# Optimization experiments

Hardware: AMD Instinct MI355X
Metric: run time of the kernel (lower is better)

The kernel has to match this reference:

```python
import jax, jax.numpy as jnp
import numpy as np

B, D, K, NC, F = 2048, 256, 256, 64, 512
EPS = 1e-3           # transport_eps
TAU_MIN = 0.01
TAU_DENOM_MIN = 1e-3


def setup_inputs() -> dict:
    key = jax.random.key(0)
    ks = jax.random.split(key, 8)
    # latents strictly inside the Poincare ball (norm ~0.5 for D=256)
    z = 0.03 * jax.random.normal(ks[0], (B, D), jnp.float32)
    features = jax.random.normal(ks[1], (B, F), jnp.float32)
    # SpectralLinear params (treated as plain linear layers in the reference)
    W_qz = 0.02 * jax.random.normal(ks[2], (K, D), jnp.float32)
    b_qz = jnp.zeros((K,), jnp.float32)
    W_qf = 0.02 * jax.random.normal(ks[3], (K, F), jnp.float32)
    b_qf = jnp.zeros((K,), jnp.float32)
    # full tensorization gamma: [K, D, D]
    q_gamma = 0.02 * jax.random.normal(ks[4], (K, D, D), jnp.float32)
    chart_queries = 0.02 * jax.random.normal(ks[5], (NC, K), jnp.float32)
    return {
        "z": z, "features": features,
        "W_qz": W_qz, "b_qz": b_qz, "W_qf": W_qf, "b_qf": b_qf,
        "q_gamma": q_gamma, "chart_queries": chart_queries,
    }


def reference(z, features, W_qz, b_qz, W_qf, b_qf, q_gamma, chart_queries):
    # centers = chart_queries[:, :latent_dim] (chart_tokens=None path); D == K here
    centers = chart_queries[:, :D]                      # [NC, D]

    # ---- hyperbolic (Poincare ball) distance scores ----
    r2 = jnp.sum(z * z, axis=-1)                        # [B]
    c_sq = jnp.sum(centers * centers, axis=-1)          # [NC]
    diff = z[:, None, :] - centers[None, :, :]          # [B, NC, D]
    dist_sq = jnp.sum(diff * diff, axis=-1)             # [B, NC]
    denom = (1.0 - r2[:, None]) * (1.0 - c_sq[None, :])
    arg = 1.0 + 2.0 * dist_sq / (denom + EPS)
    dist = jnp.arccosh(jnp.maximum(arg, 1.0 + EPS))

    # metric-aware temperature tau(z)
    tau = jnp.maximum(
        jnp.sqrt(jnp.float32(K)) * jnp.maximum(1.0 - r2, TAU_DENOM_MIN) * 0.5,
        TAU_MIN,
    )                                                   # [B]
    scores = -dist / tau[:, None]                       # [B, NC]

    # ---- feature-based refinement (q_feat_proj branch) ----
    q = z @ W_qz.T + b_qz + features @ W_qf.T + b_qf    # [B, K]
    # gamma term: einsum('bij,kij->bk', z outer z, q_gamma) without [B,D,D]
    gz = jnp.einsum('bj,kij->bki', z, q_gamma)          # [B, K, D]
    q = q + jnp.einsum('bki,bi->bk', gz, z)             # [B, K]

    # transported queries: base_queries / lambda(z); (Q/lam) . q == (q @ Q.T)/lam
    r2c = jnp.minimum(r2, 1.0 - EPS)
    lam = 2.0 / (1.0 - r2c + EPS)                       # [B]
    feature_scores = (q @ chart_queries.T) / lam[:, None]  # [B, NC]

    scores = scores + 0.1 * feature_scores / tau[:, None]

    router_weights = jax.nn.softmax(scores, axis=-1)    # [B, NC]
    K_chart = jnp.argmax(router_weights, axis=-1)       # [B]
    return router_weights, K_chart
```

## Files before the change

kernel.cpp:

```cpp
#include <hip/hip_runtime.h>
#include <hip/hip_bf16.h>
#include <hip/hip_fp16.h>


#define B_SZ 2048
#define D_SZ 256
#define K_SZ 256
#define NC_SZ 64
#define F_SZ 512
#define P_SZ 65536

typedef float  floatx4  __attribute__((ext_vector_type(4)));
typedef float  floatx16 __attribute__((ext_vector_type(16)));
typedef _Float16 h8 __attribute__((ext_vector_type(8)));
typedef __fp16  fp16x2 __attribute__((ext_vector_type(2)));
union H8U4 { uint4 u; h8 h; };

#define WS_WZT   0
#define WS_WFT   16384
#define WS_BEFF  49152
#define WS_CSQ   49216
#define WS_CQT   49280
#define WS_Q2    65664
#define WS_MH    196736
#define WS_WALL  2293888
#define WS_PART  2351232

__device__ __forceinline__ unsigned pkrtz_u(float a, float b) {
    fp16x2 r = __builtin_amdgcn_cvt_pkrtz(a, b);
    return __builtin_bit_cast(unsigned, r);
}
__device__ __forceinline__ unsigned packh2(_Float16 a, _Float16 b) {
    union { _Float16 h[2]; unsigned u; } r; r.h[0] = a; r.h[1] = b; return r.u;
}
__device__ __forceinline__ unsigned packh(float a, float b) {
    return packh2((_Float16)a, (_Float16)b);
}

__device__ __forceinline__ void gload16(const void* g, void* l) {
    __builtin_amdgcn_global_load_lds(
        (const __attribute__((address_space(1))) unsigned*)g,
        (__attribute__((address_space(3))) unsigned*)l, 16, 0, 0);
}

__global__ __launch_bounds__(256) void prep_kernel(
        const float* __restrict__ Wqz, const float* __restrict__ bqz,
        const float* __restrict__ Wqf, const float* __restrict__ bqf,
        const float* __restrict__ cq,  float* __restrict__ ws) {
    const int tid = threadIdx.x;
    const int w = tid >> 6, c = tid & 63;
    const int bid = blockIdx.x;

    if (bid >= 193) {
        _Float16* cqh = (_Float16*)(ws + WS_Q2);
        const int idx = (bid - 193)*256 + tid;
        const floatx4* sp = (const floatx4*)(cq + idx*8);
        floatx4 a = sp[0], b = sp[1];
        uint4 u = { pkrtz_u(a[0],a[1]), pkrtz_u(a[2],a[3]),
                    pkrtz_u(b[0],b[1]), pkrtz_u(b[2],b[3]) };
        *(uint4*)(cqh + idx*8) = u;
        return;
    }

    __shared__ float cqL[64*257];
    #pragma unroll
    for (int s = 0; s < 16; ++s) {
        const int e4 = s*256 + tid;
        const int row = e4 >> 6, col = (e4 & 63)*4;
        floatx4 v = *(const floatx4*)(cq + e4*4);
        #pragma unroll
        for (int u = 0; u < 4; ++u) cqL[row*257 + col + u] = v[u];
    }
    __syncthreads();

    if (bid < 64) {
        const int i = bid*4 + w;
        float a0 = 0.f, a1 = 0.f, a2 = 0.f, a3 = 0.f;
        #pragma unroll 8
        for (int k = 0; k < K_SZ; k += 4) {
            a0 = fmaf(cqL[c*257 + k    ], Wqz[(k    )*D_SZ + i], a0);
            a1 = fmaf(cqL[c*257 + k + 1], Wqz[(k + 1)*D_SZ + i], a1);
            a2 = fmaf(cqL[c*257 + k + 2], Wqz[(k + 2)*D_SZ + i], a2);
            a3 = fmaf(cqL[c*257 + k + 3], Wqz[(k + 3)*D_SZ + i], a3);
        }
        ws[WS_WZT + i*64 + c] = (a0 + a1) + (a2 + a3);
        ws[WS_CQT + i*64 + c] = cqL[c*257 + i];
    } else if (bid < 192) {
        const int j = (bid - 64)*4 + w;
        float a0 = 0.f, a1 = 0.f, a2 = 0.f, a3 = 0.f;
        #pragma unroll 8
        for (int k = 0; k < K_SZ; k += 4) {
            a0 = fmaf(cqL[c*257 + k    ], Wqf[(k    )*F_SZ + j], a0);
            a1 = fmaf(cqL[c*257 + k + 1], Wqf[(k + 1)*F_SZ + j], a1);
            a2 = fmaf(cqL[c*257 + k + 2], Wqf[(k + 2)*F_SZ + j], a2);
            a3 = fmaf(cqL[c*257 + k + 3], Wqf[(k + 3)*F_SZ + j], a3);
        }
        ws[WS_WFT + j*64 + c] = (a0 + a1) + (a2 + a3);
    } else {
        if (w == 0) {
            float acc = 0.f;
            for (int k = 0; k < K_SZ; ++k)
                acc = fmaf(cqL[c*257 + k], bqz[k] + bqf[k], acc);
            ws[WS_BEFF + c] = acc;
        } else if (w == 1) {
            float acc = 0.f;
            for (int i = 0; i < D_SZ; ++i) {
                const float v = cqL[c*257 + i];
                acc = fmaf(v, v, acc);
            }
            ws[WS_CSQ + c] = acc;
        }
    }
}

__global__ __launch_bounds__(256) void prep2_kernel(float* __restrict__ ws) {
    const int gi = blockIdx.x*256 + threadIdx.x;
    const int s  = gi >> 11, e = gi & 2047;
    const int cr = e >> 5,  u = e & 31;
    const float* __restrict__ src =
        (s == 0) ? ws + WS_WZT :
        (s <= 2) ? ws + WS_WFT :
        (s <= 4) ? ws + WS_WFT + 16384 : ws + WS_CQT;
    const bool lo = (s == 2) || (s == 4) || (s == 6);
    float v[8];
    #pragma unroll
    for (int off = 0; off < 8; ++off)
        v[off] = src[(u*8 + off)*64 + cr];
    uint4 o;
    if (!lo) {
        o.x = packh(v[0], v[1]); o.y = packh(v[2], v[3]);
        o.z = packh(v[4], v[5]); o.w = packh(v[6], v[7]);
    } else {
        float l[8];
        #pragma unroll
        for (int off = 0; off < 8; ++off) {
            const _Float16 h = (_Float16)v[off];
            l[off] = (v[off] - (float)h) * 1024.f;
        }
        o.x = pkrtz_u(l[0], l[1]); o.y = pkrtz_u(l[2], l[3]);
        o.z = pkrtz_u(l[4], l[5]); o.w = pkrtz_u(l[6], l[7]);
    }
    char* wall = (char*)(ws + WS_WALL);
    *(uint4*)(wall + s*32768 + cr*512 + ((u ^ (cr & 31)) << 4)) = o;
}

__global__ __launch_bounds__(256, 4) void mc_kernel(
        const float* __restrict__ gamma, const _Float16* __restrict__ cqh,
        _Float16* __restrict__ mh) {
    const int tid = threadIdx.x;
    const int w = tid >> 6, lane = tid & 63;
    const int ln = lane & 31, half = lane >> 5;
    const int mt = w >> 1, ns = w & 1;
    const int p0 = blockIdx.x * 64;
    const int iseg = p0 >> 8, j0 = p0 & 255;

    floatx16 acc;
    #pragma unroll
    for (int r = 0; r < 16; ++r) acc[r] = 0.f;

    const int arow = mt*32 + ln;
    const float* __restrict__ gbase = gamma + (size_t)(half*8)*P_SZ + p0 + ns*32 + ln;

    #pragma unroll 2
    for (int kc = 0; kc < 16; ++kc) {
        float g[8];
        #pragma unroll
        for (int kk = 0; kk < 8; ++kk)
            g[kk] = gbase[(size_t)(kc*16 + kk)*P_SZ];
        H8U4 a; a.u = *(const uint4*)(cqh + arow*256 + kc*16 + half*8);
        H8U4 b;
        b.u.x = pkrtz_u(g[0], g[1]);
        b.u.y = pkrtz_u(g[2], g[3]);
        b.u.z = pkrtz_u(g[4], g[5]);
        b.u.w = pkrtz_u(g[6], g[7]);
        acc = __builtin_amdgcn_mfma_f32_32x32x16_f16(a.h, b.h, acc, 0, 0, 0);
    }
    #pragma unroll
    for (int r = 0; r < 16; ++r) {
        const int cc = mt*32 + (r&3) + 8*(r>>2) + 4*half;
        const int j  = j0 + ns*32 + ln;
        const int jc = j >> 3, off = j & 7;
        mh[(size_t)cc*P_SZ + iseg*256 + ((jc ^ (cc&31))*8 + off)] = (_Float16)acc[r];
    }
}

__global__ __launch_bounds__(256) void qf_kernel(
        const float* __restrict__ z, const _Float16* __restrict__ mh,
        float* __restrict__ part) {
    __shared__ __align__(16) char bt[2][64 * 512];
    const int tid = threadIdx.x;
    const int w = tid >> 6, lane = tid & 63;
    const int ln = lane & 31, half = lane >> 5;
    const int b0 = blockIdx.x * 128;
    const int ig = blockIdx.y;
    const int bb = b0 + w*32 + ln;

    #define STAGE(i, sel)                                                     \
        _Pragma("unroll")                                                     \
        for (int s = 0; s < 8; ++s) {                                         \
            const int e = s*256 + tid;                                        \
            gload16((const char*)mh +                                         \
                    ((size_t)(e >> 5)*P_SZ + (size_t)(i)*256)*2 + (e & 31)*16,\
                    bt[sel] + e*16);                                          \
        }

    STAGE(ig*8, 0);

    uint4 zjh[16];
    #pragma unroll
    for (int ch = 0; ch < 16; ++ch) {
        const floatx4* zp = (const floatx4*)(z + bb*D_SZ + ch*16 + half*8);
        floatx4 a = zp[0], b = zp[1];
        zjh[ch].x = pkrtz_u(a[0], a[1]);
        zjh[ch].y = pkrtz_u(a[2], a[3]);
        zjh[ch].z = pkrtz_u(b[0], b[1]);
        zjh[ch].w = pkrtz_u(b[2], b[3]);
    }
    float ziv[8];
    {
        const floatx4* zp = (const floatx4*)(z + bb*D_SZ + ig*8);
        floatx4 a = zp[0], b = zp[1];
        #pragma unroll
        for (int t = 0; t < 4; ++t) { ziv[t] = a[t]; ziv[4+t] = b[t]; }
    }

    floatx16 acc0, acc1;
    #pragma unroll
    for (int r = 0; r < 16; ++r) { acc0[r] = 0.f; acc1[r] = 0.f; }

    for (int il = 0; il < 8; ++il) {
        __syncthreads();
        if (il < 7) { STAGE(ig*8 + il + 1, (il + 1) & 1); }

        const float zi = ziv[il];
        const unsigned zu = pkrtz_u(zi, zi);
        H8U4 zb; zb.u.x = zu; zb.u.y = zu; zb.u.z = zu; zb.u.w = zu;
        const char* btc = bt[il & 1];
        __builtin_amdgcn_s_setprio(1);
        #pragma unroll
        for (int ch = 0; ch < 16; ++ch) {
            H8U4 aj; aj.u = zjh[ch];
            h8 af = aj.h * zb.h;
            const int pc = ((ch*2 + half) ^ ln) * 16;
            H8U4 f0, f1;
            f0.u = *(const uint4*)(btc + ln*512 + pc);
            f1.u = *(const uint4*)(btc + (32 + ln)*512 + pc);
            acc0 = __builtin_amdgcn_mfma_f32_32x32x16_f16(af, f0.h, acc0, 0, 0, 0);
            acc1 = __builtin_amdgcn_mfma_f32_32x32x16_f16(af, f1.h, acc1, 0, 0, 0);
        }
        __builtin_amdgcn_s_setprio(0);
    }
    #undef STAGE

    float* __restrict__ qp = part + (size_t)ig * (B_SZ * NC_SZ);
    #pragma unroll
    for (int r = 0; r < 16; ++r) {
        const int row  = (r&3) + 8*(r>>2) + 4*half;
        const int brow = b0 + w*32 + row;
        qp[brow*NC_SZ + ln]      = acc0[r];
        qp[brow*NC_SZ + 32 + ln] = acc1[r];
    }
}

__global__ __launch_bounds__(256) void lin2_kernel(
        const float* __restrict__ z, const float* __restrict__ feat,
        const float* __restrict__ wall_f, float* __restrict__ part,
        float* __restrict__ dot) {
    __shared__ __align__(16) char bt[2][64 * 512];
    const char* wall = (const char*)wall_f;
    const int tid = threadIdx.x;
    const int w = tid >> 6, lane = tid & 63;
    const int ln = lane & 31, half = lane >> 5;
    const int b0 = blockIdx.x * 128;
    const int s  = blockIdx.y;
    const int bb = b0 + w*32 + ln;
    const int s_hi = (s == 0) ? 0 : (s == 1) ? 1 : (s == 2) ? 3 : 5;

    #pragma unroll
    for (int e0 = 0; e0 < 8; ++e0) {
        const int e = e0*256 + tid;
        gload16(wall + s_hi*32768 + e*16, bt[0] + e*16);
    }
    if (s > 0) {
        #pragma unroll
        for (int e0 = 0; e0 < 8; ++e0) {
            const int e = e0*256 + tid;
            gload16(wall + (s_hi + 1)*32768 + e*16, bt[1] + e*16);
        }
    }
    const float* __restrict__ arow =
        (s == 0 || s == 3) ? z + bb*D_SZ : feat + bb*F_SZ + (s == 2 ? 256 : 0);
    __syncthreads();

    floatx16 hh0, hh1, lh0, lh1, hl0, hl1;
    #pragma unroll
    for (int r = 0; r < 16; ++r) {
        hh0[r] = 0.f; hh1[r] = 0.f; lh0[r] = 0.f;
        lh1[r] = 0.f; hl0[r] = 0.f; hl1[r] = 0.f;
    }

    #pragma unroll
    for (int ch = 0; ch < 16; ++ch) {
        const floatx4* ap = (const floatx4*)(arow + ch*16 + half*8);
        floatx4 a4 = ap[0], b4 = ap[1];
        float vv[8];
        #pragma unroll
        for (int t = 0; t < 4; ++t) { vv[t] = a4[t]; vv[4+t] = b4[t]; }
        _Float16 hc[8];
        #pragma unroll
        for (int j = 0; j < 8; ++j) hc[j] = (_Float16)vv[j];
        H8U4 ah;
        ah.u.x = packh2(hc[0], hc[1]); ah.u.y = packh2(hc[2], hc[3]);
        ah.u.z = packh2(hc[4], hc[5]); ah.u.w = packh2(hc[6], hc[7]);

        const int pc = ((ch*2 + half) ^ ln) * 16;
        H8U4 f0, f1;
        f0.u = *(const uint4*)(bt[0] + ln*512 + pc);
        f1.u = *(const uint4*)(bt[0] + (32 + ln)*512 + pc);
        hh0 = __builtin_amdgcn_mfma_f32_32x32x16_f16(ah.h, f0.h, hh0, 0, 0, 0);
        hh1 = __builtin_amdgcn_mfma_f32_32x32x16_f16(ah.h, f1.h, hh1, 0, 0, 0);

        if (s > 0) {
            float l[8];
            #pragma unroll
            for (int j = 0; j < 8; ++j) l[j] = (vv[j] - (float)hc[j]) * 1024.f;
            H8U4 al;
            al.u.x = pkrtz_u(l[0], l[1]); al.u.y = pkrtz_u(l[2], l[3]);
            al.u.z = pkrtz_u(l[4], l[5]); al.u.w = pkrtz_u(l[6], l[7]);
            H8U4 g0, g1;
            g0.u = *(const uint4*)(bt[1] + ln*512 + pc);
            g1.u = *(const uint4*)(bt[1] + (32 + ln)*512 + pc);
            lh0 = __builtin_amdgcn_mfma_f32_32x32x16_f16(al.h, f0.h, lh0, 0, 0, 0);
            lh1 = __builtin_amdgcn_mfma_f32_32x32x16_f16(al.h, f1.h, lh1, 0, 0, 0);
            hl0 = __builtin_amdgcn_mfma_f32_32x32x16_f16(ah.h, g0.h, hl0, 0, 0, 0);
            hl1 = __builtin_amdgcn_mfma_f32_32x32x16_f16(ah.h, g1.h, hl1, 0, 0, 0);
        }
    }

    const float is = 1.0f / 1024.0f;
    float* __restrict__ qp = part + (size_t)(32 + s) * (B_SZ * NC_SZ);
    #pragma unroll
    for (int r = 0; r < 16; ++r) {
        const int row  = (r&3) + 8*(r>>2) + 4*half;
        const int brow = b0 + w*32 + row;
        float v0 = hh0[r], v1 = hh1[r];
        if (s > 0) { v0 += (lh0[r] + hl0[r])*is; v1 += (lh1[r] + hl1[r])*is; }
        if (s < 3) {
            qp[brow*NC_SZ + ln]      = v0;
            qp[brow*NC_SZ + 32 + ln] = v1;
        } else {
            dot[brow*NC_SZ + ln]      = v0;
            dot[brow*NC_SZ + 32 + ln] = v1;
        }
    }
}

__global__ __launch_bounds__(256) void final_kernel(
        const float* __restrict__ z, const float* __restrict__ ws,
        const float* __restrict__ dot, float* __restrict__ out) {
    const int w = threadIdx.x >> 6, c = threadIdx.x & 63;
    const int b = blockIdx.x*4 + w;

    const floatx4 zv = *(const floatx4*)(z + b*D_SZ + c*4);
    float r2 = zv[0]*zv[0] + zv[1]*zv[1] + zv[2]*zv[2] + zv[3]*zv[3];
    #pragma unroll
    for (int off = 32; off > 0; off >>= 1)
        r2 += __shfl_xor(r2, off, 64);

    const float* __restrict__ part = ws + WS_PART;
    float Q = ws[WS_BEFF + c];
    #pragma unroll
    for (int p = 0; p < 35; ++p)
        Q += part[(size_t)p * (B_SZ*NC_SZ) + b*NC_SZ + c];

    const float csq = ws[WS_CSQ + c];
    const float dsq = fmaf(-2.f, dot[b*64 + c], r2) + csq;

    const double r2d = (double)r2, csqd = (double)csq, dsqd = (double)dsq;
    const double denom = (1.0 - r2d) * (1.0 - csqd);
    double arg = 1.0 + 2.0 * dsqd / (denom + 0.001);
    if (arg < 1.001) arg = 1.001;
    const double dist = acosh(arg);
    double tmp = 1.0 - r2d; if (tmp < 0.001) tmp = 0.001;
    double tau = 8.0 * tmp;
    if (tau < 0.01) tau = 0.01;
    double r2c = r2d; if (r2c > 0.999) r2c = 0.999;
    const double lam = 2.0 / (1.0 - r2c + 0.001);
    const double score = -dist / tau + 0.1 * ((double)Q / lam) / tau;

    double m = score;
    #pragma unroll
    for (int off = 32; off > 0; off >>= 1) {
        double o = __shfl_xor(m, off, 64);
        m = fmax(m, o);
    }
    const double e = exp(score - m);
    double s = e;
    #pragma unroll
    for (int off = 32; off > 0; off >>= 1) s += __shfl_xor(s, off, 64);
    out[b*NC_SZ + c] = (float)(e / s);

    double bsc = score; int bix = c;
    #pragma unroll
    for (int off = 32; off > 0; off >>= 1) {
        double osc = __shfl_xor(bsc, off, 64);
        int    oix = __shfl_xor(bix, off, 64);
        if (osc > bsc || (osc == bsc && oix < bix)) { bsc = osc; bix = oix; }
    }
    if (c == 0) out[B_SZ*NC_SZ + b] = (float)bix;
}

extern "C" void kernel_launch(void* const* d_in, const int* in_sizes, int n_in,
                              void* d_out, int out_size, void* d_ws, size_t ws_size,
                              hipStream_t stream) {
    const float* z    = (const float*)d_in[0];
    const float* feat = (const float*)d_in[1];
    const float* Wqz  = (const float*)d_in[2];
    const float* bqz  = (const float*)d_in[3];
    const float* Wqf  = (const float*)d_in[4];
    const float* bqf  = (const float*)d_in[5];
    const float* gamma= (const float*)d_in[6];
    const float* cq   = (const float*)d_in[7];
    float* out = (float*)d_out;
    float* ws  = (float*)d_ws;
    _Float16* cqh = (_Float16*)(ws + WS_Q2);
    _Float16* mh  = (_Float16*)(ws + WS_MH);
    float*    dot = ws + WS_MH;

    prep_kernel<<<201, 256, 0, stream>>>(Wqz, bqz, Wqf, bqf, cq, ws);
    prep2_kernel<<<56, 256, 0, stream>>>(ws);
    mc_kernel<<<1024, 256, 0, stream>>>(gamma, cqh, mh);
    qf_kernel<<<dim3(16, 32), 256, 0, stream>>>(z, mh, ws + WS_PART);
    lin2_kernel<<<dim3(16, 4), 256, 0, stream>>>(z, feat, ws + WS_WALL,
                                                 ws + WS_PART, dot);
    final_kernel<<<512, 256, 0, stream>>>(z, ws, dot, out);
}
```

Before: 177.0 us.

## Fuse fp16 weight packing into prep kernel and remap blocks for XCD locality

Removes the prep2 kernel by having prep_kernel write the fp16 hi/lo split, swizzled weight layout straight into the WALL buffer, which saves a launch and a round trip through the fp32 intermediates. The mc_kernel K-loop now starts at a per-block rotated offset so concurrent blocks spread their gamma reads across different rows. qf_kernel switches to a 1D grid mapped so blocks sharing an i-group land on the same XCD, aiming for better L2 reuse of mh tiles. The fused writes are scattered 2-byte stores instead of packed 16-byte stores.

```diff
diff --git a/kernel.cpp b/kernel.cpp
--- a/kernel.cpp
+++ b/kernel.cpp
@@ -16,11 +16,8 @@
 typedef __fp16  fp16x2 __attribute__((ext_vector_type(2)));
 union H8U4 { uint4 u; h8 h; };
 
-#define WS_WZT   0
-#define WS_WFT   16384
 #define WS_BEFF  49152
 #define WS_CSQ   49216
-#define WS_CQT   49280
 #define WS_Q2    65664
 #define WS_MH    196736
 #define WS_WALL  2293888
@@ -30,11 +27,12 @@
     fp16x2 r = __builtin_amdgcn_cvt_pkrtz(a, b);
     return __builtin_bit_cast(unsigned, r);
 }
+__device__ __forceinline__ _Float16 h16rtz(float x) {
+    fp16x2 r = __builtin_amdgcn_cvt_pkrtz(x, x);
+    return (_Float16)r[0];
+}
 __device__ __forceinline__ unsigned packh2(_Float16 a, _Float16 b) {
     union { _Float16 h[2]; unsigned u; } r; r.h[0] = a; r.h[1] = b; return r.u;
-}
-__device__ __forceinline__ unsigned packh(float a, float b) {
-    return packh2((_Float16)a, (_Float16)b);
 }
 
 __device__ __forceinline__ void gload16(const void* g, void* l) {
@@ -50,6 +48,7 @@
     const int tid = threadIdx.x;
     const int w = tid >> 6, c = tid & 63;
     const int bid = blockIdx.x;
+    char* wall = (char*)(ws + WS_WALL);
 
     if (bid >= 193) {
         _Float16* cqh = (_Float16*)(ws + WS_Q2);
@@ -83,8 +82,14 @@
             a2 = fmaf(cqL[c*257 + k + 2], Wqz[(k + 2)*D_SZ + i], a2);
             a3 = fmaf(cqL[c*257 + k + 3], Wqz[(k + 3)*D_SZ + i], a3);
         }
-        ws[WS_WZT + i*64 + c] = (a0 + a1) + (a2 + a3);
-        ws[WS_CQT + i*64 + c] = cqL[c*257 + i];
+        const float acc = (a0 + a1) + (a2 + a3);
+        const int boff = c*512 + ((((i >> 3) & 31) ^ (c & 31)) << 4) + (i & 7)*2;
+        *(_Float16*)(wall + 0*32768 + boff) = (_Float16)acc;
+        const float v = cqL[c*257 + i];
+        const _Float16 vh = (_Float16)v;
+        *(_Float16*)(wall + 5*32768 + boff) = vh;
+        *(_Float16*)(wall + 6*32768 + boff) =
+            h16rtz((v - (float)vh) * 1024.f);
     } else if (bid < 192) {
         const int j = (bid - 64)*4 + w;
         float a0 = 0.f, a1 = 0.f, a2 = 0.f, a3 = 0.f;
@@ -95,7 +100,14 @@
             a2 = fmaf(cqL[c*257 + k + 2], Wqf[(k + 2)*F_SZ + j], a2);
             a3 = fmaf(cqL[c*257 + k + 3], Wqf[(k + 3)*F_SZ + j], a3);
         }
-        ws[WS_WFT + j*64 + c] = (a0 + a1) + (a2 + a3);
+        const float acc = (a0 + a1) + (a2 + a3);
+        const int row = j & 255;
+        const int sbase = (j < 256) ? 1 : 3;
+        const int boff = c*512 + ((((row >> 3) & 31) ^ (c & 31)) << 4) + (row & 7)*2;
+        const _Float16 ah = (_Float16)acc;
+        *(_Float16*)(wall + (size_t)sbase*32768 + boff) = ah;
+        *(_Float16*)(wall + (size_t)(sbase + 1)*32768 + boff) =
+            h16rtz((acc - (float)ah) * 1024.f);
     } else {
         if (w == 0) {
             float acc = 0.f;
@@ -113,37 +125,6 @@
     }
 }
 
-__global__ __launch_bounds__(256) void prep2_kernel(float* __restrict__ ws) {
-    const int gi = blockIdx.x*256 + threadIdx.x;
-    const int s  = gi >> 11, e = gi & 2047;
-    const int cr = e >> 5,  u = e & 31;
-    const float* __restrict__ src =
-        (s == 0) ? ws + WS_WZT :
-        (s <= 2) ? ws + WS_WFT :
-        (s <= 4) ? ws + WS_WFT + 16384 : ws + WS_CQT;
-    const bool lo = (s == 2) || (s == 4) || (s == 6);
-    float v[8];
-    #pragma unroll
-    for (int off = 0; off < 8; ++off)
-        v[off] = src[(u*8 + off)*64 + cr];
-    uint4 o;
-    if (!lo) {
-        o.x = packh(v[0], v[1]); o.y = packh(v[2], v[3]);
-        o.z = packh(v[4], v[5]); o.w = packh(v[6], v[7]);
-    } else {
-        float l[8];
-        #pragma unroll
-        for (int off = 0; off < 8; ++off) {
-            const _Float16 h = (_Float16)v[off];
-            l[off] = (v[off] - (float)h) * 1024.f;
-        }
-        o.x = pkrtz_u(l[0], l[1]); o.y = pkrtz_u(l[2], l[3]);
-        o.z = pkrtz_u(l[4], l[5]); o.w = pkrtz_u(l[6], l[7]);
-    }
-    char* wall = (char*)(ws + WS_WALL);
-    *(uint4*)(wall + s*32768 + cr*512 + ((u ^ (cr & 31)) << 4)) = o;
-}
-
 __global__ __launch_bounds__(256, 4) void mc_kernel(
         const float* __restrict__ gamma, const _Float16* __restrict__ cqh,
         _Float16* __restrict__ mh) {
@@ -153,6 +134,7 @@
     const int mt = w >> 1, ns = w & 1;
     const int p0 = blockIdx.x * 64;
     const int iseg = p0 >> 8, j0 = p0 & 255;
+    const int rot = blockIdx.x & 15;
 
     floatx16 acc;
     #pragma unroll
@@ -162,7 +144,8 @@
     const float* __restrict__ gbase = gamma + (size_t)(half*8)*P_SZ + p0 + ns*32 + ln;
 
     #pragma unroll 2
-    for (int kc = 0; kc < 16; ++kc) {
+    for (int t = 0; t < 16; ++t) {
+        const int kc = (t + rot) & 15;
         float g[8];
         #pragma unroll
         for (int kk = 0; kk < 8; ++kk)
@@ -191,8 +174,11 @@
     const int tid = threadIdx.x;
     const int w = tid >> 6, lane = tid & 63;
     const int ln = lane & 31, half = lane >> 5;
-    const int b0 = blockIdx.x * 128;
-    const int ig = blockIdx.y;
+    const int bid = blockIdx.x;
+    const int xcd = bid & 7;
+    const int y   = bid >> 3;
+    const int ig  = xcd*4 + (y & 3);
+    const int b0  = (y >> 2) * 128;
     const int bb = b0 + w*32 + ln;
 
     #define STAGE(i, sel)                                                     \
@@ -428,9 +414,8 @@
     float*    dot = ws + WS_MH;
 
     prep_kernel<<<201, 256, 0, stream>>>(Wqz, bqz, Wqf, bqf, cq, ws);
-    prep2_kernel<<<56, 256, 0, stream>>>(ws);
     mc_kernel<<<1024, 256, 0, stream>>>(gamma, cqh, mh);
-    qf_kernel<<<dim3(16, 32), 256, 0, stream>>>(z, mh, ws + WS_PART);
+    qf_kernel<<<512, 256, 0, stream>>>(z, mh, ws + WS_PART);
     lin2_kernel<<<dim3(16, 4), 256, 0, stream>>>(z, feat, ws + WS_WALL,
                                                  ws + WS_PART, dot);
     final_kernel<<<512, 256, 0, stream>>>(z, ws, dot, out);
```

New measurement: 179.2 us. About the same (+1.2%).
